# Optimization experiments

Hardware: AMD Instinct MI355X
Metric: run time of the kernel (lower is better)

## Reference

```python
import jax, jax.numpy as jnp
import numpy as np
from functools import partial

H = 64  # hidden_size
F = 5   # num_features
ALPHA_RANK = 1.0
NEG_SLOPE = 0.2


def setup_inputs() -> dict:
    key = jax.random.key(0)
    ks = jax.random.split(key, 10)
    N, T = 4096, 512
    feature = jax.random.normal(ks[0], (N, T, F), dtype=jnp.float32)
    ret = jax.random.normal(ks[1], (N,), dtype=jnp.float32)
    mask = jax.random.bernoulli(ks[2], 0.9, (N,))
    s = 1.0 / np.sqrt(H)
    Wih = jax.random.uniform(ks[3], (4 * H, F), jnp.float32, -s, s)
    Whh = jax.random.uniform(ks[4], (4 * H, H), jnp.float32, -s, s)
    bih = jax.random.uniform(ks[5], (4 * H,), jnp.float32, -s, s)
    bhh = jax.random.uniform(ks[6], (4 * H,), jnp.float32, -s, s)
    Wd = jax.random.uniform(ks[7], (1, H), jnp.float32, -s, s)
    bd = jax.random.uniform(ks[8], (1,), jnp.float32, -s, s)
    return {"feature": feature, "ret": ret, "mask": mask,
            "Wih": Wih, "Whh": Whh, "bih": bih, "bhh": bhh,
            "Wd": Wd, "bd": bd}


def _lstm_last_h(x, Wih, Whh, bih, bhh):
    # x: [N, T, F] -> last hidden state [N, H]. PyTorch gate order: i, f, g, o.
    N = x.shape[0]
    b = bih + bhh
    # precompute input projections for all steps: [T, N, 4H]
    x_proj = jnp.einsum('ntf,gf->tng', x, Wih) + b

    def step(carry, xt):
        h, c = carry
        gates = xt + h @ Whh.T  # [N, 4H]
        i, f, g, o = jnp.split(gates, 4, axis=-1)
        i = jax.nn.sigmoid(i)
        f = jax.nn.sigmoid(f)
        g = jnp.tanh(g)
        o = jax.nn.sigmoid(o)
        c = f * c + i * g
        h = o * jnp.tanh(c)
        return (h, c), None

    h0 = jnp.zeros((N, H), x.dtype)
    c0 = jnp.zeros((N, H), x.dtype)
    (h, _), _ = jax.lax.scan(step, (h0, c0), x_proj)
    return h


def _masked_mse(pred, gt, mask):
    m = mask.astype(pred.dtype)
    return jnp.sum((pred - gt) ** 2 * m) / (jnp.sum(m) + 1e-8)


def _rank_loss(pred, gt, mask):
    m = mask.astype(pred.dtype)
    pred_diff = pred[None, :] - pred[:, None]   # [i,j] = pred[j]-pred[i]
    true_diff = gt[None, :] - gt[:, None]
    mm = m[None, :] * m[:, None]
    return jnp.mean(jax.nn.relu(-pred_diff * true_diff * mm))


def reference(feature, ret, mask, Wih, Whh, bih, bhh, Wd, bd):
    h_last = _lstm_last_h(feature, Wih, Whh, bih, bhh)          # [N, H]
    pred = jax.nn.leaky_relu(h_last @ Wd.T + bd, NEG_SLOPE)[:, 0]  # [N]
    reg_loss = _masked_mse(pred, ret, mask)
    rank_loss = _rank_loss(pred, ret, mask)
    loss = reg_loss + ALPHA_RANK * rank_loss
    return pred, loss, reg_loss, rank_loss
```

## Files before the change

kernel.cpp:

```cpp
#include <hip/hip_runtime.h>

#define NSEQ   4096
#define TSTEPS 512
#define FIN    5
#define HID    64
#define SPB    16
#define BLK    512

typedef __attribute__((ext_vector_type(8))) short bsh8;
typedef __attribute__((ext_vector_type(4))) float f32x4;
typedef __attribute__((ext_vector_type(4))) int   i32x4;

#define MFMA16(A, B, C) __builtin_amdgcn_mfma_f32_16x16x32_bf16((A), (B), (C), 0, 0, 0)

#define LOG2E 1.4426950408889634f
#define SNEG  (-LOG2E)
#define SPOS  (2.0f * LOG2E)

struct Frag2 { bsh8 hi; bsh8 lo; };

__device__ __forceinline__ unsigned short bf16hi_rn(float x) {
    unsigned u = __float_as_uint(x);
    return (unsigned short)((u + 0x7fffu + ((u >> 16) & 1u)) >> 16);
}
__device__ __forceinline__ void split_bf16(float v, unsigned short& h, unsigned short& l) {
    h = bf16hi_rn(v);
    float hf_ = __uint_as_float(((unsigned)h) << 16);
    l = bf16hi_rn(v - hf_);
}
__device__ __forceinline__ float rcp1pexp2(float x) {
    return __builtin_amdgcn_rcpf(1.0f + __builtin_amdgcn_exp2f(x));
}

__device__ __forceinline__ Frag2 load_whh_frag(const float* __restrict__ Whh, int row, int k, float scale) {
    const float* p = Whh + row * HID + k;
    Frag2 r;
#pragma unroll
    for (int j = 0; j < 8; ++j) {
        unsigned short h, l;
        split_bf16(scale * p[j], h, l);
        r.hi[j] = (short)h; r.lo[j] = (short)l;
    }
    return r;
}
__device__ __forceinline__ Frag2 load_wih_frag(const float* __restrict__ Wih,
                                               const float* __restrict__ bih,
                                               const float* __restrict__ bhh,
                                               int row, int quad, float scale) {
    Frag2 r;
#pragma unroll
    for (int j = 0; j < 8; ++j) { r.hi[j] = 0; r.lo[j] = 0; }
    if (quad == 0) {
        unsigned short h, l;
#pragma unroll
        for (int j = 0; j < FIN; ++j) {
            split_bf16(scale * Wih[row * FIN + j], h, l);
            r.hi[j] = (short)h; r.lo[j] = (short)l;
        }
        split_bf16(scale * (bih[row] + bhh[row]), h, l);
        r.hi[FIN] = (short)h; r.lo[FIN] = (short)l;
    }
    return r;
}

__device__ __forceinline__ void stage_chunk(const float* __restrict__ feat,
                                            bsh8 (*dst)[SPB],
                                            int seq0, int t0, int tidE) {
#pragma unroll
    for (int it = 0; it < (64 * SPB) / 256; ++it) {
        int idx = tidE + it * 256;
        int t2  = idx >> 4;
        int s   = idx & 15;
        const float* xp = feat + (size_t)(seq0 + s) * (TSTEPS * FIN) + (t0 + t2) * FIN;
        bsh8 v = {0, 0, 0, 0, 0, 0, 0, 0};
#pragma unroll
        for (int j = 0; j < FIN; ++j) v[j] = (short)bf16hi_rn(xp[j]);
        v[FIN] = (short)0x3F80;
        dst[t2][s] = v;
    }
}

__global__ __launch_bounds__(BLK)
void lstm_kernel(const float* __restrict__ feat,
                 const float* __restrict__ Wih,
                 const float* __restrict__ Whh,
                 const float* __restrict__ bih,
                 const float* __restrict__ bhh,
                 const float* __restrict__ Wd,
                 const float* __restrict__ bd,
                 float* __restrict__ pred,
                 float* __restrict__ accums) {
    __shared__ bsh8  aA[2][SPB][9];
    __shared__ bsh8  xb[2][64][SPB];
    __shared__ __align__(16) float seedb[2][4][HID][SPB];
    __shared__ float hf[SPB][HID + 1];
    __shared__ float pf[SPB][17];

    const int tid   = threadIdx.x;
    const int w     = tid >> 6;
    const int lane  = tid & 63;
    const int col   = lane & 15;
    const int quad  = lane >> 4;
    const int quad4 = quad * 4;
    const int seq0  = blockIdx.x * SPB;

    if (blockIdx.x == 0 && tid < 4) accums[tid] = 0.0f;

    {
        bsh8 z = {0, 0, 0, 0, 0, 0, 0, 0};
        if (tid < SPB * 9) (&aA[0][0][0])[tid] = z;
    }
    if (w >= 4) stage_chunk(feat, xb[0], seq0, 0, tid - 256);
    __syncthreads();

    if (w < 4) {
        const int u = 16 * w + col;
        const Frag2 b00 = load_whh_frag(Whh, 0*HID + u,      quad*8, SNEG);
        const Frag2 b01 = load_whh_frag(Whh, 0*HID + u, 32 + quad*8, SNEG);
        const Frag2 b10 = load_whh_frag(Whh, 1*HID + u,      quad*8, SNEG);
        const Frag2 b11 = load_whh_frag(Whh, 1*HID + u, 32 + quad*8, SNEG);
        const Frag2 b20 = load_whh_frag(Whh, 2*HID + u,      quad*8, SPOS);
        const Frag2 b21 = load_whh_frag(Whh, 2*HID + u, 32 + quad*8, SPOS);
        const Frag2 b30 = load_whh_frag(Whh, 3*HID + u,      quad*8, SNEG);
        const Frag2 b31 = load_whh_frag(Whh, 3*HID + u, 32 + quad*8, SNEG);

        float cs_[4] = {0.f, 0.f, 0.f, 0.f};
        __builtin_amdgcn_s_setprio(1);

        for (int t = 0; t < TSTEPS; ++t) {
            const int buf = t & 1;
            const int nb  = buf ^ 1;
            __syncthreads();

            f32x4 acc0 = *(const f32x4*)&seedb[buf][0][u][quad4];
            f32x4 acc1 = *(const f32x4*)&seedb[buf][1][u][quad4];
            f32x4 acc2 = *(const f32x4*)&seedb[buf][2][u][quad4];
            f32x4 acc3 = *(const f32x4*)&seedb[buf][3][u][quad4];
            bsh8 ah0 = aA[buf][col][quad];
            bsh8 ah1 = aA[buf][col][4 + quad];

            acc0 = MFMA16(ah0, b00.hi, acc0); acc0 = MFMA16(ah1, b01.hi, acc0);
            acc1 = MFMA16(ah0, b10.hi, acc1); acc1 = MFMA16(ah1, b11.hi, acc1);
            acc2 = MFMA16(ah0, b20.hi, acc2); acc2 = MFMA16(ah1, b21.hi, acc2);
            acc3 = MFMA16(ah0, b30.hi, acc3); acc3 = MFMA16(ah1, b31.hi, acc3);
            acc0 = MFMA16(ah0, b00.lo, acc0); acc0 = MFMA16(ah1, b01.lo, acc0);
            acc1 = MFMA16(ah0, b10.lo, acc1); acc1 = MFMA16(ah1, b11.lo, acc1);
            acc2 = MFMA16(ah0, b20.lo, acc2); acc2 = MFMA16(ah1, b21.lo, acc2);
            acc3 = MFMA16(ah0, b30.lo, acc3); acc3 = MFMA16(ah1, b31.lo, acc3);

            float hh_[4];
#pragma unroll
            for (int r = 0; r < 4; ++r) {
                float si  = rcp1pexp2(acc0[r]);
                float sf  = rcp1pexp2(acc1[r]);
                float rg  = rcp1pexp2(acc2[r]);
                float so  = rcp1pexp2(acc3[r]);
                float tgK = __builtin_fmaf(-2.0f * SPOS, rg, SPOS);
                cs_[r] = __builtin_fmaf(sf, cs_[r], si * tgK);
                float rc  = rcp1pexp2(cs_[r]);
                float t2  = so * rc;
                hh_[r] = __builtin_fmaf(-2.0f, t2, so);
            }
            unsigned pk01, pk23;
            asm("v_cvt_pk_bf16_f32 %0, %1, %2" : "=v"(pk01) : "v"(hh_[0]), "v"(hh_[1]));
            asm("v_cvt_pk_bf16_f32 %0, %1, %2" : "=v"(pk23) : "v"(hh_[2]), "v"(hh_[3]));
            unsigned short* hp = (unsigned short*)&aA[nb][quad4][0] + u;
            hp[0]   = (unsigned short)pk01;
            hp[72]  = (unsigned short)(pk01 >> 16);
            hp[144] = (unsigned short)pk23;
            hp[216] = (unsigned short)(pk23 >> 16);
            if (t == TSTEPS - 1) {
                hf[quad4 + 0][u] = hh_[0];
                hf[quad4 + 1][u] = hh_[1];
                hf[quad4 + 2][u] = hh_[2];
                hf[quad4 + 3][u] = hh_[3];
            }
        }
        __builtin_amdgcn_s_setprio(0);
    } else {
        const int wE   = w - 4;
        const int uE   = 16 * wE + col;
        const int tidE = tid - 256;
        const Frag2 w0 = load_wih_frag(Wih, bih, bhh, 0*HID + uE, quad, SNEG);
        const Frag2 w1 = load_wih_frag(Wih, bih, bhh, 1*HID + uE, quad, SNEG);
        const Frag2 w2 = load_wih_frag(Wih, bih, bhh, 2*HID + uE, quad, SPOS);
        const Frag2 w3 = load_wih_frag(Wih, bih, bhh, 3*HID + uE, quad, SNEG);

        {
            bsh8 ax = xb[0][0][col];
            f32x4 e0 = {0.f,0.f,0.f,0.f}, e1 = e0, e2 = e0, e3 = e0;
            e0 = MFMA16(ax, w0.hi, e0); e0 = MFMA16(ax, w0.lo, e0);
            e1 = MFMA16(ax, w1.hi, e1); e1 = MFMA16(ax, w1.lo, e1);
            e2 = MFMA16(ax, w2.hi, e2); e2 = MFMA16(ax, w2.lo, e2);
            e3 = MFMA16(ax, w3.hi, e3); e3 = MFMA16(ax, w3.lo, e3);
            *(f32x4*)&seedb[0][0][uE][quad4] = e0;
            *(f32x4*)&seedb[0][1][uE][quad4] = e1;
            *(f32x4*)&seedb[0][2][uE][quad4] = e2;
            *(f32x4*)&seedb[0][3][uE][quad4] = e3;
        }
        for (int t = 0; t < TSTEPS; ++t) {
            __syncthreads();
            if ((t & 63) == 0 && t + 64 < TSTEPS)
                stage_chunk(feat, xb[((t >> 6) + 1) & 1], seq0, ((t >> 6) + 1) * 64, tidE);
            if (t + 1 < TSTEPS) {
                const int t1 = t + 1;
                bsh8 ax = xb[(t1 >> 6) & 1][t1 & 63][col];
                f32x4 e0 = {0.f,0.f,0.f,0.f}, e1 = e0, e2 = e0, e3 = e0;
                e0 = MFMA16(ax, w0.hi, e0); e0 = MFMA16(ax, w0.lo, e0);
                e1 = MFMA16(ax, w1.hi, e1); e1 = MFMA16(ax, w1.lo, e1);
                e2 = MFMA16(ax, w2.hi, e2); e2 = MFMA16(ax, w2.lo, e2);
                e3 = MFMA16(ax, w3.hi, e3); e3 = MFMA16(ax, w3.lo, e3);
                const int sb = t1 & 1;
                *(f32x4*)&seedb[sb][0][uE][quad4] = e0;
                *(f32x4*)&seedb[sb][1][uE][quad4] = e1;
                *(f32x4*)&seedb[sb][2][uE][quad4] = e2;
                *(f32x4*)&seedb[sb][3][uE][quad4] = e3;
            }
        }
    }
    __syncthreads();

    if (tid < 256) {
        int s  = tid & 15;
        int hq = tid >> 4;
        int j0 = hq * 4;
        float part = hf[s][j0] * Wd[j0] + hf[s][j0 + 1] * Wd[j0 + 1]
                   + hf[s][j0 + 2] * Wd[j0 + 2] + hf[s][j0 + 3] * Wd[j0 + 3];
        pf[s][hq] = part;
    }
    __syncthreads();
    if (tid < SPB) {
        float sum = bd[0];
#pragma unroll
        for (int j = 0; j < 16; ++j) sum += pf[tid][j];
        float p = (sum >= 0.0f) ? sum : 0.2f * sum;
        pred[seq0 + tid] = p;
    }
}

__global__ __launch_bounds__(256)
void loss_kernel(const float* __restrict__ pred,
                 const float* __restrict__ ret,
                 const int* __restrict__ mask,
                 float* __restrict__ accums) {
    __shared__ __align__(16) float sp[NSEQ];
    __shared__ __align__(16) float sg[NSEQ];
    __shared__ __align__(16) float sq[NSEQ];
    __shared__ float wsum[8];
    int tid = threadIdx.x;
    for (int idx = tid; idx < NSEQ / 4; idx += 256) {
        f32x4 p4 = ((const f32x4*)pred)[idx];
        f32x4 g4 = ((const f32x4*)ret)[idx];
        i32x4 m4 = ((const i32x4*)mask)[idx];
        f32x4 q4;
#pragma unroll
        for (int l = 0; l < 4; ++l) q4[l] = m4[l] ? 1.0f : 0.0f;
        *(f32x4*)&sp[idx * 4] = p4;
        *(f32x4*)&sg[idx * 4] = g4;
        *(f32x4*)&sq[idx * 4] = q4;
    }
    __syncthreads();

    if (blockIdx.x == 0) {
        float v = 0.0f, m = 0.0f;
        for (int j = tid; j < NSEQ; j += 256) {
            float mj = sq[j];
            float d  = sp[j] - sg[j];
            v += d * d * mj;
            m += mj;
        }
#pragma unroll
        for (int off = 32; off > 0; off >>= 1) {
            v += __shfl_down(v, off, 64);
            m += __shfl_down(m, off, 64);
        }
        if ((tid & 63) == 0) {
            atomicAdd(&accums[0], v);
            atomicAdd(&accums[1], m);
        }
    }

    int iloc = tid >> 5;
    int jp   = tid & 31;
    int i    = blockIdx.x * 8 + iloc;
    float pi = sp[i], gi = sg[i], qi = sq[i];
    float sum = 0.0f;
    for (int j0 = jp * 4; j0 < NSEQ; j0 += 128) {
        f32x4 p4 = *(const f32x4*)&sp[j0];
        f32x4 g4 = *(const f32x4*)&sg[j0];
        f32x4 q4 = *(const f32x4*)&sq[j0];
#pragma unroll
        for (int l = 0; l < 4; ++l) {
            float t = -(p4[l] - pi) * (g4[l] - gi);
            sum += fmaxf(t, 0.0f) * q4[l];
        }
    }
    sum *= qi;
#pragma unroll
    for (int off = 16; off > 0; off >>= 1) sum += __shfl_down(sum, off, 32);
    if (jp == 0) wsum[iloc] = sum;
    __syncthreads();
    if (tid == 0) {
        float s = wsum[0] + wsum[1] + wsum[2] + wsum[3]
                + wsum[4] + wsum[5] + wsum[6] + wsum[7];
        atomicAdd(&accums[2], s);
    }
}

__global__ void final_kernel(const float* __restrict__ accums,
                             float* __restrict__ out) {
    float reg  = accums[0] / (accums[1] + 1e-8f);
    float rank = accums[2] / 16777216.0f;
    out[NSEQ + 0] = reg + rank;
    out[NSEQ + 1] = reg;
    out[NSEQ + 2] = rank;
}

extern "C" void kernel_launch(void* const* d_in, const int* in_sizes, int n_in,
                              void* d_out, int out_size, void* d_ws, size_t ws_size,
                              hipStream_t stream) {
    const float* feat = (const float*)d_in[0];
    const float* ret  = (const float*)d_in[1];
    const int*   mask = (const int*)d_in[2];
    const float* Wih  = (const float*)d_in[3];
    const float* Whh  = (const float*)d_in[4];
    const float* bih  = (const float*)d_in[5];
    const float* bhh  = (const float*)d_in[6];
    const float* Wd   = (const float*)d_in[7];
    const float* bd   = (const float*)d_in[8];
    float* out    = (float*)d_out;
    float* accums = (float*)d_ws;

    lstm_kernel<<<NSEQ / SPB, BLK, 0, stream>>>(feat, Wih, Whh, bih, bhh,
                                                Wd, bd, out, accums);
    loss_kernel<<<NSEQ / 8, 256, 0, stream>>>(out, ret, mask, accums);
    final_kernel<<<1, 1, 0, stream>>>(accums, out);
}
```

Before: 365.6 us.

## Merge gate reciprocals, decouple seed loads from MFMA chain, relayout seed buffer

Rewrites the LSTM cell activations so paired sigmoid/tanh terms share a single reciprocal (i with g, o with c), which removes two of the five transcendental reciprocals per element. The MFMA chain now starts from zero accumulators and adds the input-projection seeds at the end, so the LDS seed loads no longer sit on the critical path before the first MFMA. The seed buffer is relaid out as per-wave, per-lane f32x4 slots, giving conflict-free contiguous LDS reads and writes. Merging the reciprocals risks overflow of the exp products for large gate pre-activations, and the final four vector adds are extra work.

```diff
diff --git a/kernel.cpp b/kernel.cpp
--- a/kernel.cpp
+++ b/kernel.cpp
@@ -27,9 +27,6 @@
     h = bf16hi_rn(v);
     float hf_ = __uint_as_float(((unsigned)h) << 16);
     l = bf16hi_rn(v - hf_);
-}
-__device__ __forceinline__ float rcp1pexp2(float x) {
-    return __builtin_amdgcn_rcpf(1.0f + __builtin_amdgcn_exp2f(x));
 }
 
 __device__ __forceinline__ Frag2 load_whh_frag(const float* __restrict__ Whh, int row, int k, float scale) {
@@ -92,7 +89,7 @@
                  float* __restrict__ accums) {
     __shared__ bsh8  aA[2][SPB][9];
     __shared__ bsh8  xb[2][64][SPB];
-    __shared__ __align__(16) float seedb[2][4][HID][SPB];
+    __shared__ __align__(16) f32x4 seedb[2][4][4][64];
     __shared__ float hf[SPB][HID + 1];
     __shared__ float pf[SPB][17];
 
@@ -132,34 +129,49 @@
             const int nb  = buf ^ 1;
             __syncthreads();
 
-            f32x4 acc0 = *(const f32x4*)&seedb[buf][0][u][quad4];
-            f32x4 acc1 = *(const f32x4*)&seedb[buf][1][u][quad4];
-            f32x4 acc2 = *(const f32x4*)&seedb[buf][2][u][quad4];
-            f32x4 acc3 = *(const f32x4*)&seedb[buf][3][u][quad4];
             bsh8 ah0 = aA[buf][col][quad];
             bsh8 ah1 = aA[buf][col][4 + quad];
-
-            acc0 = MFMA16(ah0, b00.hi, acc0); acc0 = MFMA16(ah1, b01.hi, acc0);
-            acc1 = MFMA16(ah0, b10.hi, acc1); acc1 = MFMA16(ah1, b11.hi, acc1);
-            acc2 = MFMA16(ah0, b20.hi, acc2); acc2 = MFMA16(ah1, b21.hi, acc2);
-            acc3 = MFMA16(ah0, b30.hi, acc3); acc3 = MFMA16(ah1, b31.hi, acc3);
-            acc0 = MFMA16(ah0, b00.lo, acc0); acc0 = MFMA16(ah1, b01.lo, acc0);
-            acc1 = MFMA16(ah0, b10.lo, acc1); acc1 = MFMA16(ah1, b11.lo, acc1);
-            acc2 = MFMA16(ah0, b20.lo, acc2); acc2 = MFMA16(ah1, b21.lo, acc2);
-            acc3 = MFMA16(ah0, b30.lo, acc3); acc3 = MFMA16(ah1, b31.lo, acc3);
+            f32x4 s0 = seedb[buf][w][0][lane];
+            f32x4 s1 = seedb[buf][w][1][lane];
+            f32x4 s2 = seedb[buf][w][2][lane];
+            f32x4 s3 = seedb[buf][w][3][lane];
+
+            const f32x4 zz = {0.f, 0.f, 0.f, 0.f};
+            f32x4 acc0 = MFMA16(ah0, b00.hi, zz);
+            f32x4 acc1 = MFMA16(ah0, b10.hi, zz);
+            f32x4 acc2 = MFMA16(ah0, b20.hi, zz);
+            f32x4 acc3 = MFMA16(ah0, b30.hi, zz);
+            acc0 = MFMA16(ah1, b01.hi, acc0);
+            acc1 = MFMA16(ah1, b11.hi, acc1);
+            acc2 = MFMA16(ah1, b21.hi, acc2);
+            acc3 = MFMA16(ah1, b31.hi, acc3);
+            acc0 = MFMA16(ah0, b00.lo, acc0);
+            acc1 = MFMA16(ah0, b10.lo, acc1);
+            acc2 = MFMA16(ah0, b20.lo, acc2);
+            acc3 = MFMA16(ah0, b30.lo, acc3);
+            acc0 = MFMA16(ah1, b01.lo, acc0);
+            acc1 = MFMA16(ah1, b11.lo, acc1);
+            acc2 = MFMA16(ah1, b21.lo, acc2);
+            acc3 = MFMA16(ah1, b31.lo, acc3);
+            acc0 = acc0 + s0;
+            acc1 = acc1 + s1;
+            acc2 = acc2 + s2;
+            acc3 = acc3 + s3;
 
             float hh_[4];
 #pragma unroll
             for (int r = 0; r < 4; ++r) {
-                float si  = rcp1pexp2(acc0[r]);
-                float sf  = rcp1pexp2(acc1[r]);
-                float rg  = rcp1pexp2(acc2[r]);
-                float so  = rcp1pexp2(acc3[r]);
-                float tgK = __builtin_fmaf(-2.0f * SPOS, rg, SPOS);
-                cs_[r] = __builtin_fmaf(sf, cs_[r], si * tgK);
-                float rc  = rcp1pexp2(cs_[r]);
-                float t2  = so * rc;
-                hh_[r] = __builtin_fmaf(-2.0f, t2, so);
+                float Ei = __builtin_amdgcn_exp2f(acc0[r]);
+                float Ef = __builtin_amdgcn_exp2f(acc1[r]);
+                float Eg = __builtin_amdgcn_exp2f(acc2[r]);
+                float Eo = __builtin_amdgcn_exp2f(acc3[r]);
+                float R1 = __builtin_amdgcn_rcpf((1.0f + Ei) * (1.0f + Eg));
+                float sf = __builtin_amdgcn_rcpf(1.0f + Ef);
+                float n1 = __builtin_fmaf(SPOS, Eg, -SPOS);
+                cs_[r] = __builtin_fmaf(sf, cs_[r], n1 * R1);
+                float Ec = __builtin_amdgcn_exp2f(cs_[r]);
+                float R2 = __builtin_amdgcn_rcpf((1.0f + Eo) * (1.0f + Ec));
+                hh_[r] = (Ec - 1.0f) * R2;
             }
             unsigned pk01, pk23;
             asm("v_cvt_pk_bf16_f32 %0, %1, %2" : "=v"(pk01) : "v"(hh_[0]), "v"(hh_[1]));
@@ -179,8 +191,8 @@
         __builtin_amdgcn_s_setprio(0);
     } else {
         const int wE   = w - 4;
+        const int tidE = tid - 256;
         const int uE   = 16 * wE + col;
-        const int tidE = tid - 256;
         const Frag2 w0 = load_wih_frag(Wih, bih, bhh, 0*HID + uE, quad, SNEG);
         const Frag2 w1 = load_wih_frag(Wih, bih, bhh, 1*HID + uE, quad, SNEG);
         const Frag2 w2 = load_wih_frag(Wih, bih, bhh, 2*HID + uE, quad, SPOS);
@@ -193,10 +205,10 @@
             e1 = MFMA16(ax, w1.hi, e1); e1 = MFMA16(ax, w1.lo, e1);
             e2 = MFMA16(ax, w2.hi, e2); e2 = MFMA16(ax, w2.lo, e2);
             e3 = MFMA16(ax, w3.hi, e3); e3 = MFMA16(ax, w3.lo, e3);
-            *(f32x4*)&seedb[0][0][uE][quad4] = e0;
-            *(f32x4*)&seedb[0][1][uE][quad4] = e1;
-            *(f32x4*)&seedb[0][2][uE][quad4] = e2;
-            *(f32x4*)&seedb[0][3][uE][quad4] = e3;
+            seedb[0][wE][0][lane] = e0;
+            seedb[0][wE][1][lane] = e1;
+            seedb[0][wE][2][lane] = e2;
+            seedb[0][wE][3][lane] = e3;
         }
         for (int t = 0; t < TSTEPS; ++t) {
             __syncthreads();
@@ -211,10 +223,10 @@
                 e2 = MFMA16(ax, w2.hi, e2); e2 = MFMA16(ax, w2.lo, e2);
                 e3 = MFMA16(ax, w3.hi, e3); e3 = MFMA16(ax, w3.lo, e3);
                 const int sb = t1 & 1;
-                *(f32x4*)&seedb[sb][0][uE][quad4] = e0;
-                *(f32x4*)&seedb[sb][1][uE][quad4] = e1;
-                *(f32x4*)&seedb[sb][2][uE][quad4] = e2;
-                *(f32x4*)&seedb[sb][3][uE][quad4] = e3;
+                seedb[sb][wE][0][lane] = e0;
+                seedb[sb][wE][1][lane] = e1;
+                seedb[sb][wE][2][lane] = e2;
+                seedb[sb][wE][3][lane] = e3;
             }
         }
     }
```

After: 351.1 us. 4.0% less time.
